# Kernel tuning notes

Measured on AMD Instinct MI355X. Metric: run time of the kernel, lower is better.

Reference implementation:

```python
import jax, jax.numpy as jnp
import numpy as np

L, B, D = 2048, 8, 1024
EPS = 1e-5  # torch LayerNorm default


def setup_inputs() -> dict:
    key = jax.random.key(0)
    k1, k2 = jax.random.split(key)
    x = jax.random.normal(k1, (L, B, D), dtype=jnp.float32)
    c = jnp.zeros((B, D), dtype=jnp.float32)
    W_ufr = 0.02 * jax.random.normal(k2, (3 * D, D), dtype=jnp.float32)
    ln_gamma = jnp.ones((D,), dtype=jnp.float32)
    ln_beta = jnp.zeros((D,), dtype=jnp.float32)
    return {"x": x, "c": c, "W_ufr": W_ufr, "ln_gamma": ln_gamma, "ln_beta": ln_beta}


def reference(x, c, W_ufr, ln_gamma, ln_beta):
    # LayerNorm over last dim
    mean = jnp.mean(x, axis=-1, keepdims=True)
    var = jnp.mean(jnp.square(x - mean), axis=-1, keepdims=True)
    x_norm = (x - mean) * jax.lax.rsqrt(var + EPS) * ln_gamma + ln_beta

    # Linear (no bias): [L,B,D] @ [D,3D]
    ufr = jnp.einsum('lbd,ed->lbe', x_norm, W_ufr)
    u, f, r = jnp.split(ufr, 3, axis=-1)
    f_gate = jax.nn.sigmoid(f)
    r_gate = jax.nn.sigmoid(r)

    # Sequential recurrence: c_t = f_t * c_{t-1} + (1 - f_t) * u_t
    def step(c_prev, fu):
        f_t, u_t = fu
        c_t = f_t * c_prev + (1.0 - f_t) * u_t
        return c_t, c_t

    last_c, c_stack = jax.lax.scan(step, c, (f_gate, u))

    hs = r_gate * jnp.tanh(c_stack) + (1.0 - r_gate) * x_norm
    return x + hs, last_c
```

## Files before the change

kernel.cpp:

```cpp
#include <hip/hip_runtime.h>
#include <hip/hip_bf16.h>
#include <stdint.h>

#define L_DIM 2048
#define B_DIM 8
#define D_DIM 1024
#define M_DIM (L_DIM * B_DIM)
#define N_DIM (3 * D_DIM)
#define K_DIM D_DIM
#define CH    (B_DIM * D_DIM)
#define EPSLN 1e-5f
#define NC 128
#define CL (L_DIM / NC)

#define BM 256
#define BN 256
#define BK 64
#define NT (K_DIM / BK)
#define GX (N_DIM / BN)
#define GY (M_DIM / BM)
#define NWG (GX * GY)

typedef __attribute__((ext_vector_type(8))) short short8;
typedef __attribute__((ext_vector_type(4))) float floatx4;

static __device__ __forceinline__ float bf16_lo(unsigned int p) {
    union { unsigned int u; float f; } v; v.u = p << 16; return v.f;
}
static __device__ __forceinline__ float bf16_hi(unsigned int p) {
    union { unsigned int u; float f; } v; v.u = p & 0xffff0000u; return v.f;
}
static __device__ __forceinline__ unsigned short f32_to_bf16(float f) {
    union { float f; unsigned int u; } v;
    v.f = f;
    unsigned int u = v.u;
    u += 0x7fffu + ((u >> 16) & 1u);
    return (unsigned short)(u >> 16);
}
static __device__ __forceinline__ float sigmoidf_fast(float v) {
    return 1.0f / (1.0f + __expf(-v));
}
static __device__ __forceinline__ float tanhf_fast(float c) {
    return 1.0f - 2.0f / (1.0f + __expf(2.0f * c));
}

static __device__ __forceinline__ void async16(const void* g, void* l) {
    __builtin_amdgcn_global_load_lds(
        (const __attribute__((address_space(1))) unsigned int*)g,
        (__attribute__((address_space(3))) unsigned int*)l,
        16, 0, 0);
}

__global__ __launch_bounds__(256) void ln_kernel(const float* __restrict__ x,
                                                 const float* __restrict__ gamma,
                                                 const float* __restrict__ beta,
                                                 unsigned short* __restrict__ xn,
                                                 float* __restrict__ meanOut,
                                                 float* __restrict__ rstdOut) {
    const int row = blockIdx.x;
    const int tid = threadIdx.x;
    const float4* xr = (const float4*)(x + (size_t)row * D_DIM);
    float4 v = xr[tid];
    float s  = v.x + v.y + v.z + v.w;
    float s2 = v.x * v.x + v.y * v.y + v.z * v.z + v.w * v.w;
    #pragma unroll
    for (int o = 32; o > 0; o >>= 1) {
        s  += __shfl_xor(s, o, 64);
        s2 += __shfl_xor(s2, o, 64);
    }
    __shared__ float red[8];
    const int wid = tid >> 6;
    if ((tid & 63) == 0) { red[wid] = s; red[4 + wid] = s2; }
    __syncthreads();
    s  = red[0] + red[1] + red[2] + red[3];
    s2 = red[4] + red[5] + red[6] + red[7];
    const float mean = s * (1.0f / D_DIM);
    const float var  = s2 * (1.0f / D_DIM) - mean * mean;
    const float rstd = rsqrtf(var + EPSLN);
    if (tid == 0) { meanOut[row] = mean; rstdOut[row] = rstd; }
    const int col = tid * 4;
    const float4 g = *(const float4*)(gamma + col);
    const float4 b = *(const float4*)(beta + col);
    unsigned short o0 = f32_to_bf16((v.x - mean) * rstd * g.x + b.x);
    unsigned short o1 = f32_to_bf16((v.y - mean) * rstd * g.y + b.y);
    unsigned short o2 = f32_to_bf16((v.z - mean) * rstd * g.z + b.z);
    unsigned short o3 = f32_to_bf16((v.w - mean) * rstd * g.w + b.w);
    uint2 packed;
    packed.x = (unsigned int)o0 | ((unsigned int)o1 << 16);
    packed.y = (unsigned int)o2 | ((unsigned int)o3 << 16);
    *(uint2*)(xn + (size_t)row * D_DIM + col) = packed;
}

__global__ __launch_bounds__(256) void wconv_kernel(const float* __restrict__ W,
                                                    unsigned short* __restrict__ Wb) {
    const size_t i = ((size_t)blockIdx.x * 256 + threadIdx.x) * 4;
    float4 v = *(const float4*)(W + i);
    uint2 packed;
    packed.x = (unsigned int)f32_to_bf16(v.x) | ((unsigned int)f32_to_bf16(v.y) << 16);
    packed.y = (unsigned int)f32_to_bf16(v.z) | ((unsigned int)f32_to_bf16(v.w) << 16);
    *(uint2*)(Wb + i) = packed;
}

__global__ __launch_bounds__(512, 2) void gemm_kernel(const unsigned short* __restrict__ A,
                                                      const unsigned short* __restrict__ W,
                                                      unsigned short* __restrict__ u,
                                                      unsigned short* __restrict__ f,
                                                      unsigned short* __restrict__ r) {
    __shared__ __align__(16) unsigned short ldsA[2][BM * BK];
    __shared__ __align__(16) unsigned short ldsB[2][BM * BK];

    const int tid  = threadIdx.x;
    const int wave = tid >> 6;
    const int lane = tid & 63;
    const int quad = lane >> 4;
    const int l16  = lane & 15;
    const int wr   = wave >> 2;
    const int wc   = wave & 3;

    const int orig = blockIdx.y * GX + blockIdx.x;
    const int swz  = (orig & 7) * (NWG / 8) + (orig >> 3);
    const int tx   = swz % GX;
    const int ty   = swz / GX;
    const int m0   = ty * BM;
    const int n0   = tx * BN;

    const int rS = tid >> 3;
    const int kS = ((tid & 7) ^ (rS & 7)) * 8;
    const unsigned short* gA = A + (size_t)(m0 + rS) * K_DIM + kS;
    const unsigned short* gB = W + (size_t)(n0 + rS) * K_DIM + kS;

    const int px     = l16 & 7;
    const int p0_8   = (quad ^ px) * 8;
    const int p1_8   = ((quad + 4) ^ px) * 8;
    const int l16_64 = l16 * 64;
    const int wr4096 = wr * 4096;
    const int wc2048 = wc * 2048;

    floatx4 acc[2][2][4][2] = {};
    short8 a[4][2];
    short8 b[2][2][2];

#define STAGE_A(B_, KT_, H_) do { \
    async16(gA + (size_t)((H_) * 128) * K_DIM + (size_t)(KT_) * 64, \
            &ldsA[B_][(H_) * 8192 + (size_t)tid * 8]); \
    async16(gA + (size_t)((H_) * 128 + 64) * K_DIM + (size_t)(KT_) * 64, \
            &ldsA[B_][(H_) * 8192 + 4096 + (size_t)tid * 8]); \
} while (0)

#define STAGE_B(B_, KT_, H_) do { \
    async16(gB + (size_t)((H_) * 128) * K_DIM + (size_t)(KT_) * 64, \
            &ldsB[B_][(H_) * 8192 + (size_t)tid * 8]); \
    async16(gB + (size_t)((H_) * 128 + 64) * K_DIM + (size_t)(KT_) * 64, \
            &ldsB[B_][(H_) * 8192 + 4096 + (size_t)tid * 8]); \
} while (0)

#define RD_A(MH_) do { \
    const unsigned short* pa_ = &ldsA[buf][(MH_) * 8192 + wr4096 + l16_64]; \
    _Pragma("unroll") \
    for (int i_ = 0; i_ < 4; i_++) { \
        a[i_][0] = *(const short8*)(pa_ + i_ * 1024 + p0_8); \
        a[i_][1] = *(const short8*)(pa_ + i_ * 1024 + p1_8); \
    } \
} while (0)

#define RD_B(NH_) do { \
    const unsigned short* pb_ = &ldsB[buf][(NH_) * 8192 + wc2048 + l16_64]; \
    _Pragma("unroll") \
    for (int j_ = 0; j_ < 2; j_++) { \
        b[NH_][j_][0] = *(const short8*)(pb_ + j_ * 1024 + p0_8); \
        b[NH_][j_][1] = *(const short8*)(pb_ + j_ * 1024 + p1_8); \
    } \
} while (0)

#define MFMA_Q(MH_, NH_) do { \
    __builtin_amdgcn_s_setprio(1); \
    _Pragma("unroll") \
    for (int i_ = 0; i_ < 4; i_++) { \
        _Pragma("unroll") \
        for (int j_ = 0; j_ < 2; j_++) { \
            acc[MH_][NH_][i_][j_] = __builtin_amdgcn_mfma_f32_16x16x32_bf16( \
                a[i_][0], b[NH_][j_][0], acc[MH_][NH_][i_][j_], 0, 0, 0); \
            acc[MH_][NH_][i_][j_] = __builtin_amdgcn_mfma_f32_16x16x32_bf16( \
                a[i_][1], b[NH_][j_][1], acc[MH_][NH_][i_][j_], 0, 0, 0); \
        } \
    } \
    __builtin_amdgcn_s_setprio(0); \
} while (0)

#define TILE_SYNC do { \
    asm volatile("s_waitcnt vmcnt(0)" ::: "memory"); \
    __builtin_amdgcn_s_barrier(); \
    __builtin_amdgcn_sched_barrier(0); \
} while (0)

    STAGE_A(0, 0, 0); STAGE_B(0, 0, 0);
    STAGE_A(0, 0, 1); STAGE_B(0, 0, 1);
    TILE_SYNC;

    for (int kt = 0; kt < NT - 1; ++kt) {
        const int buf  = kt & 1;
        const int nbuf = buf ^ 1;
        STAGE_A(nbuf, kt + 1, 0); STAGE_B(nbuf, kt + 1, 0);
        STAGE_A(nbuf, kt + 1, 1); STAGE_B(nbuf, kt + 1, 1);
        RD_A(0); RD_B(0);
        MFMA_Q(0, 0);
        RD_B(1);
        MFMA_Q(0, 1);
        RD_A(1);
        MFMA_Q(1, 1);
        MFMA_Q(1, 0);
        TILE_SYNC;
    }

    {
        const int buf = (NT - 1) & 1;
        RD_A(0); RD_B(0);
        MFMA_Q(0, 0);
        RD_B(1);
        MFMA_Q(0, 1);
        RD_A(1);
        MFMA_Q(1, 1);
        MFMA_Q(1, 0);
    }

#undef TILE_SYNC
#undef MFMA_Q
#undef RD_A
#undef RD_B
#undef STAGE_A
#undef STAGE_B

    const int region = n0 >> 10;
    const int nnb = n0 & 1023;
    unsigned short* dst = (region == 0) ? u : ((region == 1) ? f : r);
    const bool sig = (region != 0);
    #pragma unroll
    for (int mh = 0; mh < 2; mh++) {
        #pragma unroll
        for (int nh = 0; nh < 2; nh++) {
            #pragma unroll
            for (int i = 0; i < 4; i++) {
                #pragma unroll
                for (int j = 0; j < 2; j++) {
                    #pragma unroll
                    for (int t = 0; t < 4; t++) {
                        const int gm = m0 + mh * 128 + wr * 64 + i * 16 + quad * 4 + t;
                        const int nn = nnb + nh * 128 + wc * 32 + j * 16 + l16;
                        float v = acc[mh][nh][i][j][t];
                        if (sig) v = sigmoidf_fast(v);
                        dst[(size_t)gm * D_DIM + nn] = f32_to_bf16(v);
                    }
                }
            }
        }
    }
}

__global__ __launch_bounds__(256) void scan_reduce(const unsigned short* __restrict__ f,
                                                   const unsigned short* __restrict__ u,
                                                   float* __restrict__ Ac,
                                                   float* __restrict__ bc) {
    const int ch2   = (blockIdx.x * 256 + threadIdx.x) * 2;
    const int chunk = blockIdx.y;
    const size_t base = (size_t)chunk * CL * CH + ch2;
    float A0 = 1.0f, b0 = 0.0f, A1 = 1.0f, b1 = 0.0f;
    #pragma unroll
    for (int i = 0; i < CL; i++) {
        const size_t idx = base + (size_t)i * CH;
        const unsigned int fp = *(const unsigned int*)(f + idx);
        const unsigned int up = *(const unsigned int*)(u + idx);
        const float f0 = bf16_lo(fp), f1 = bf16_hi(fp);
        const float u0 = bf16_lo(up), u1 = bf16_hi(up);
        b0 = f0 * (b0 - u0) + u0;
        b1 = f1 * (b1 - u1) + u1;
        A0 *= f0;
        A1 *= f1;
    }
    *(float2*)(Ac + chunk * CH + ch2) = make_float2(A0, A1);
    *(float2*)(bc + chunk * CH + ch2) = make_float2(b0, b1);
}

__global__ __launch_bounds__(256) void scan_spine(const float* __restrict__ Ac,
                                                  const float* __restrict__ bc,
                                                  const float* __restrict__ c0,
                                                  float* __restrict__ cst) {
    const int ch = blockIdx.x * 256 + threadIdx.x;
    float c = c0[ch];
    #pragma unroll 16
    for (int j = 0; j < NC; j++) {
        cst[j * CH + ch] = c;
        c = Ac[j * CH + ch] * c + bc[j * CH + ch];
    }
}

__global__ __launch_bounds__(256) void scan_apply(const unsigned short* __restrict__ f,
                                                  const unsigned short* __restrict__ u,
                                                  const unsigned short* __restrict__ r,
                                                  const float* __restrict__ x,
                                                  const float* __restrict__ meanIn,
                                                  const float* __restrict__ rstdIn,
                                                  const float* __restrict__ gamma,
                                                  const float* __restrict__ beta,
                                                  const float* __restrict__ cst,
                                                  float* __restrict__ out,
                                                  float* __restrict__ lastc) {
    const int ch2   = (blockIdx.x * 256 + threadIdx.x) * 2;
    const int chunk = blockIdx.y;
    const int bidx  = ch2 >> 10;
    const int d     = ch2 & 1023;
    const float2 g  = *(const float2*)(gamma + d);
    const float2 be = *(const float2*)(beta + d);
    const size_t base = (size_t)chunk * CL * CH + ch2;
    float2 cc = *(const float2*)(cst + chunk * CH + ch2);
    float c0v = cc.x, c1v = cc.y;
    #pragma unroll 4
    for (int i = 0; i < CL; i++) {
        const int rowLB = (chunk * CL + i) * B_DIM + bidx;
        const float mu = meanIn[rowLB];
        const float rs = rstdIn[rowLB];
        const size_t idx = base + (size_t)i * CH;
        const unsigned int fp = *(const unsigned int*)(f + idx);
        const unsigned int up = *(const unsigned int*)(u + idx);
        const unsigned int rp = *(const unsigned int*)(r + idx);
        const float2 xv = *(const float2*)(x + idx);
        const float f0 = bf16_lo(fp), f1 = bf16_hi(fp);
        const float u0 = bf16_lo(up), u1 = bf16_hi(up);
        c0v = f0 * (c0v - u0) + u0;
        c1v = f1 * (c1v - u1) + u1;
        const float r0 = bf16_lo(rp), r1 = bf16_hi(rp);
        const float n0 = (xv.x - mu) * rs * g.x + be.x;
        const float n1 = (xv.y - mu) * rs * g.y + be.y;
        float2 o;
        o.x = xv.x + r0 * tanhf_fast(c0v) + (1.0f - r0) * n0;
        o.y = xv.y + r1 * tanhf_fast(c1v) + (1.0f - r1) * n1;
        *(float2*)(out + idx) = o;
    }
    if (chunk == NC - 1) *(float2*)(lastc + ch2) = make_float2(c0v, c1v);
}

extern "C" void kernel_launch(void* const* d_in, const int* in_sizes, int n_in,
                              void* d_out, int out_size, void* d_ws, size_t ws_size,
                              hipStream_t stream) {
    const float* x     = (const float*)d_in[0];
    const float* c0    = (const float*)d_in[1];
    const float* W     = (const float*)d_in[2];
    const float* gamma = (const float*)d_in[3];
    const float* beta  = (const float*)d_in[4];

    float* out   = (float*)d_out;
    float* lastc = out + (size_t)M_DIM * D_DIM;

    char* ws = (char*)d_ws;
    unsigned short* xn = (unsigned short*)ws;  ws += (size_t)M_DIM * K_DIM * 2;
    unsigned short* Wb = (unsigned short*)ws;  ws += (size_t)N_DIM * K_DIM * 2;
    unsigned short* u  = (unsigned short*)ws;  ws += (size_t)M_DIM * D_DIM * 2;
    unsigned short* f  = (unsigned short*)ws;  ws += (size_t)M_DIM * D_DIM * 2;
    unsigned short* r  = (unsigned short*)ws;  ws += (size_t)M_DIM * D_DIM * 2;
    float* meanBuf = (float*)ws;               ws += (size_t)M_DIM * 4;
    float* rstdBuf = (float*)ws;               ws += (size_t)M_DIM * 4;
    float* Ac  = (float*)ws;                   ws += (size_t)NC * CH * 4;
    float* bc  = (float*)ws;                   ws += (size_t)NC * CH * 4;
    float* cst = (float*)ws;                   ws += (size_t)NC * CH * 4;

    ln_kernel<<<M_DIM, 256, 0, stream>>>(x, gamma, beta, xn, meanBuf, rstdBuf);
    wconv_kernel<<<(N_DIM * K_DIM) / 1024, 256, 0, stream>>>(W, Wb);
    gemm_kernel<<<dim3(GX, GY), 512, 0, stream>>>(xn, Wb, u, f, r);
    scan_reduce<<<dim3(CH / 512, NC), 256, 0, stream>>>(f, u, Ac, bc);
    scan_spine<<<CH / 256, 256, 0, stream>>>(Ac, bc, c0, cst);
    scan_apply<<<dim3(CH / 512, NC), 256, 0, stream>>>(f, u, r, x, meanBuf, rstdBuf,
                                                       gamma, beta, cst, out, lastc);
}
```

Measured before the change: 302.0 us.

## Software-pipeline LDS fragment reads across the tile barrier in bf16 GEMM

Restructures the GEMM main loop into finer MFMA groups that work on half-size A fragments, using ping-pong register sets. The first A and B fragments of the next K tile are read right after the barrier and overlap the remaining MFMAs, so the MFMA pipe is not left idle waiting for LDS reads at each tile start. The tile barrier now sits in the middle of the loop body. This costs extra fragment registers and a more complex schedule, with some risk of register pressure or spills under launch bounds of 512 threads and 2 blocks.

```diff
diff --git a/kernel.cpp b/kernel.cpp
--- a/kernel.cpp
+++ b/kernel.cpp
@@ -106,8 +106,8 @@
                                                       unsigned short* __restrict__ u,
                                                       unsigned short* __restrict__ f,
                                                       unsigned short* __restrict__ r) {
-    __shared__ __align__(16) unsigned short ldsA[2][BM * BK];
-    __shared__ __align__(16) unsigned short ldsB[2][BM * BK];
+    __shared__ __align__(16) unsigned short ldsA[2 * BM * BK];
+    __shared__ __align__(16) unsigned short ldsB[2 * BM * BK];
 
     const int tid  = threadIdx.x;
     const int wave = tid >> 6;
@@ -137,57 +137,54 @@
     const int wc2048 = wc * 2048;
 
     floatx4 acc[2][2][4][2] = {};
-    short8 a[4][2];
-    short8 b[2][2][2];
-
-#define STAGE_A(B_, KT_, H_) do { \
+    short8 aP[2][2], aQ[2][2], b0[2][2], b1[2][2];
+
+#define STAGE_A(BO_, KT_, H_) do { \
     async16(gA + (size_t)((H_) * 128) * K_DIM + (size_t)(KT_) * 64, \
-            &ldsA[B_][(H_) * 8192 + (size_t)tid * 8]); \
+            &ldsA[(BO_) + (H_) * 8192 + (size_t)tid * 8]); \
     async16(gA + (size_t)((H_) * 128 + 64) * K_DIM + (size_t)(KT_) * 64, \
-            &ldsA[B_][(H_) * 8192 + 4096 + (size_t)tid * 8]); \
-} while (0)
-
-#define STAGE_B(B_, KT_, H_) do { \
+            &ldsA[(BO_) + (H_) * 8192 + 4096 + (size_t)tid * 8]); \
+} while (0)
+
+#define STAGE_B(BO_, KT_, H_) do { \
     async16(gB + (size_t)((H_) * 128) * K_DIM + (size_t)(KT_) * 64, \
-            &ldsB[B_][(H_) * 8192 + (size_t)tid * 8]); \
+            &ldsB[(BO_) + (H_) * 8192 + (size_t)tid * 8]); \
     async16(gB + (size_t)((H_) * 128 + 64) * K_DIM + (size_t)(KT_) * 64, \
-            &ldsB[B_][(H_) * 8192 + 4096 + (size_t)tid * 8]); \
-} while (0)
-
-#define RD_A(MH_) do { \
-    const unsigned short* pa_ = &ldsA[buf][(MH_) * 8192 + wr4096 + l16_64]; \
-    _Pragma("unroll") \
-    for (int i_ = 0; i_ < 4; i_++) { \
-        a[i_][0] = *(const short8*)(pa_ + i_ * 1024 + p0_8); \
-        a[i_][1] = *(const short8*)(pa_ + i_ * 1024 + p1_8); \
-    } \
-} while (0)
-
-#define RD_B(NH_) do { \
-    const unsigned short* pb_ = &ldsB[buf][(NH_) * 8192 + wc2048 + l16_64]; \
-    _Pragma("unroll") \
-    for (int j_ = 0; j_ < 2; j_++) { \
-        b[NH_][j_][0] = *(const short8*)(pb_ + j_ * 1024 + p0_8); \
-        b[NH_][j_][1] = *(const short8*)(pb_ + j_ * 1024 + p1_8); \
-    } \
-} while (0)
-
-#define MFMA_Q(MH_, NH_) do { \
+            &ldsB[(BO_) + (H_) * 8192 + 4096 + (size_t)tid * 8]); \
+} while (0)
+
+#define RD_A4(ARR_, BO_, MH_, IH_) do { \
+    const unsigned short* pa_ = &ldsA[(BO_) + (MH_) * 8192 + wr4096 + (IH_) * 2048 + l16_64]; \
+    ARR_[0][0] = *(const short8*)(pa_ + p0_8); \
+    ARR_[0][1] = *(const short8*)(pa_ + p1_8); \
+    ARR_[1][0] = *(const short8*)(pa_ + 1024 + p0_8); \
+    ARR_[1][1] = *(const short8*)(pa_ + 1024 + p1_8); \
+} while (0)
+
+#define RD_B4(ARR_, BO_, NH_) do { \
+    const unsigned short* pb_ = &ldsB[(BO_) + (NH_) * 8192 + wc2048 + l16_64]; \
+    ARR_[0][0] = *(const short8*)(pb_ + p0_8); \
+    ARR_[0][1] = *(const short8*)(pb_ + p1_8); \
+    ARR_[1][0] = *(const short8*)(pb_ + 1024 + p0_8); \
+    ARR_[1][1] = *(const short8*)(pb_ + 1024 + p1_8); \
+} while (0)
+
+#define OCT(ARR_, BRR_, MH_, NH_, IH_) do { \
     __builtin_amdgcn_s_setprio(1); \
     _Pragma("unroll") \
-    for (int i_ = 0; i_ < 4; i_++) { \
+    for (int il_ = 0; il_ < 2; il_++) { \
         _Pragma("unroll") \
         for (int j_ = 0; j_ < 2; j_++) { \
-            acc[MH_][NH_][i_][j_] = __builtin_amdgcn_mfma_f32_16x16x32_bf16( \
-                a[i_][0], b[NH_][j_][0], acc[MH_][NH_][i_][j_], 0, 0, 0); \
-            acc[MH_][NH_][i_][j_] = __builtin_amdgcn_mfma_f32_16x16x32_bf16( \
-                a[i_][1], b[NH_][j_][1], acc[MH_][NH_][i_][j_], 0, 0, 0); \
+            acc[MH_][NH_][(IH_)*2 + il_][j_] = __builtin_amdgcn_mfma_f32_16x16x32_bf16( \
+                ARR_[il_][0], BRR_[j_][0], acc[MH_][NH_][(IH_)*2 + il_][j_], 0, 0, 0); \
+            acc[MH_][NH_][(IH_)*2 + il_][j_] = __builtin_amdgcn_mfma_f32_16x16x32_bf16( \
+                ARR_[il_][1], BRR_[j_][1], acc[MH_][NH_][(IH_)*2 + il_][j_], 0, 0, 0); \
         } \
     } \
     __builtin_amdgcn_s_setprio(0); \
 } while (0)
 
-#define TILE_SYNC do { \
+#define TILE_BARRIER do { \
     asm volatile("s_waitcnt vmcnt(0)" ::: "memory"); \
     __builtin_amdgcn_s_barrier(); \
     __builtin_amdgcn_sched_barrier(0); \
@@ -195,40 +192,54 @@
 
     STAGE_A(0, 0, 0); STAGE_B(0, 0, 0);
     STAGE_A(0, 0, 1); STAGE_B(0, 0, 1);
-    TILE_SYNC;
+    TILE_BARRIER;
+    RD_A4(aP, 0, 0, 0);
+    RD_B4(b0, 0, 0);
 
     for (int kt = 0; kt < NT - 1; ++kt) {
-        const int buf  = kt & 1;
-        const int nbuf = buf ^ 1;
-        STAGE_A(nbuf, kt + 1, 0); STAGE_B(nbuf, kt + 1, 0);
-        STAGE_A(nbuf, kt + 1, 1); STAGE_B(nbuf, kt + 1, 1);
-        RD_A(0); RD_B(0);
-        MFMA_Q(0, 0);
-        RD_B(1);
-        MFMA_Q(0, 1);
-        RD_A(1);
-        MFMA_Q(1, 1);
-        MFMA_Q(1, 0);
-        TILE_SYNC;
+        const int bufS = (kt & 1) << 14;
+        const int nbS  = bufS ^ 16384;
+        STAGE_A(nbS, kt + 1, 0); STAGE_B(nbS, kt + 1, 0);
+        STAGE_A(nbS, kt + 1, 1); STAGE_B(nbS, kt + 1, 1);
+        RD_B4(b1, bufS, 1);
+        OCT(aP, b0, 0, 0, 0);
+        RD_A4(aQ, bufS, 0, 1);
+        OCT(aP, b1, 0, 1, 0);
+        RD_A4(aP, bufS, 1, 0);
+        OCT(aQ, b0, 0, 0, 1);
+        OCT(aQ, b1, 0, 1, 1);
+        RD_A4(aQ, bufS, 1, 1);
+        TILE_BARRIER;
+        OCT(aP, b0, 1, 0, 0);
+        OCT(aP, b1, 1, 1, 0);
+        RD_A4(aP, nbS, 0, 0);
+        OCT(aQ, b0, 1, 0, 1);
+        RD_B4(b0, nbS, 0);
+        OCT(aQ, b1, 1, 1, 1);
     }
 
     {
-        const int buf = (NT - 1) & 1;
-        RD_A(0); RD_B(0);
-        MFMA_Q(0, 0);
-        RD_B(1);
-        MFMA_Q(0, 1);
-        RD_A(1);
-        MFMA_Q(1, 1);
-        MFMA_Q(1, 0);
-    }
-
-#undef TILE_SYNC
-#undef MFMA_Q
-#undef RD_A
-#undef RD_B
+        const int bufS = 16384;
+        RD_B4(b1, bufS, 1);
+        OCT(aP, b0, 0, 0, 0);
+        RD_A4(aQ, bufS, 0, 1);
+        OCT(aP, b1, 0, 1, 0);
+        RD_A4(aP, bufS, 1, 0);
+        OCT(aQ, b0, 0, 0, 1);
+        OCT(aQ, b1, 0, 1, 1);
+        RD_A4(aQ, bufS, 1, 1);
+        OCT(aP, b0, 1, 0, 0);
+        OCT(aP, b1, 1, 1, 0);
+        OCT(aQ, b0, 1, 0, 1);
+        OCT(aQ, b1, 1, 1, 1);
+    }
+
+#undef TILE_BARRIER
+#undef OCT
+#undef RD_B4
+#undef RD_A4
+#undef STAGE_B
 #undef STAGE_A
-#undef STAGE_B
 
     const int region = n0 >> 10;
     const int nnb = n0 & 1023;
```

New measurement: 288.6 us. -4.4%, faster.
